# Optimization experiments

Hardware: AMD Instinct MI355X
Metric: run time of the kernel (lower is better)

Reference implementation:

```python
import jax, jax.numpy as jnp
import numpy as np

N = 8192
IN, HID, NH, TOT = 64, 64, 4, 128
DH = TOT // NH  # 32


def setup_inputs() -> dict:
    key = jax.random.key(0)
    ks = jax.random.split(key, 8)
    s = 0.05
    return {
        "input": jax.random.normal(ks[0], (N, IN), jnp.float32),
        "hx": jax.random.normal(ks[1], (N, HID), jnp.float32),
        "Wq": jax.random.normal(ks[2], (NH, TOT, DH), jnp.float32) * s,
        "Wk": jax.random.normal(ks[3], (NH, TOT, DH), jnp.float32) * s,
        "Wr": jax.random.normal(ks[4], (TOT, HID), jnp.float32) * s,
        "br": jnp.zeros((HID,), jnp.float32),
        "Wz": jax.random.normal(ks[5], (TOT, HID), jnp.float32) * s,
        "bz": jnp.zeros((HID,), jnp.float32),
        "Wh": jax.random.normal(ks[6], (TOT, HID), jnp.float32) * s,
        "bh": jnp.zeros((HID,), jnp.float32),
    }


def _dyn_adj(x, Wq, Wk):
    # x: [N, T]; multi-head attention adjacency, averaged over heads -> [N, N]
    q = jnp.einsum('nt,htd->hnd', x, Wq)
    k = jnp.einsum('nt,htd->hnd', x, Wk)
    scores = jnp.einsum('hnd,hmd->hnm', q, k) / jnp.sqrt(jnp.float32(DH))
    return jnp.mean(jax.nn.softmax(scores, axis=-1), axis=0)  # [N, N]


def reference(input, hx, Wq, Wk, Wr, br, Wz, bz, Wh, bh):
    x = jnp.concatenate([input, hx], axis=1)          # [N, TOT]
    adj = _dyn_adj(x, Wq, Wk)                         # [N, N] row-stochastic
    ax = adj @ x                                      # shared adjacency application
    r = jax.nn.sigmoid(ax @ Wr + br)                  # [N, HID]
    z = jax.nn.sigmoid(ax @ Wz + bz)                  # [N, HID]
    x2 = jnp.concatenate([input, r * hx], axis=1)     # [N, TOT]
    h = jnp.tanh((adj @ x2) @ Wh + bh)                # [N, HID]
    return z * hx + (1.0 - z) * h
```

## Files before the change

### kernel.cpp

```cpp
#include <hip/hip_runtime.h>
#include <hip/hip_bf16.h>

#define NN 8192
#define TOTD 128
#define HIDD 64
#define NHEAD 4
#define DHD 32
#define NCQ 8
#define JPB (NN / 32 / NCQ)

typedef __attribute__((ext_vector_type(8))) short short8;
typedef __attribute__((ext_vector_type(4))) float f32x4;

__device__ __forceinline__ short f2b(float f) {
  unsigned u = __builtin_bit_cast(unsigned, f);
  u += 0x7fff + ((u >> 16) & 1);
  return (short)(u >> 16);
}

__device__ __forceinline__ void gl_lds16(const short* g, short* l) {
  __builtin_amdgcn_global_load_lds(
      (const __attribute__((address_space(1))) void*)g,
      (__attribute__((address_space(3))) void*)l, 16, 0, 0);
}

__global__ void k_build_xfrag(const float* __restrict__ in, const float* __restrict__ hx,
                              short* __restrict__ xb) {
  int i = blockIdx.x * 256 + threadIdx.x;
  int n = i >> 7;
  int t = i & 127;
  float v = (t < 64) ? in[n * 64 + t] : hx[n * 64 + (t - 64)];
  int jt = n >> 5, kk = n & 31, cg = t >> 4;
  int l = ((kk >> 3) << 4) | (t & 15);
  xb[(((size_t)jt * 8 + cg) << 9) + (l << 3) + (kk & 7)] = f2b(v);
}

__global__ void k_qk(const float* __restrict__ in, const float* __restrict__ hx,
                     const float* __restrict__ Wq, const float* __restrict__ Wk,
                     short* __restrict__ qb, short* __restrict__ kb) {
  __shared__ float xr[TOTD];
  int n = blockIdx.x;
  int tid = threadIdx.x;
  if (tid < TOTD) xr[tid] = (tid < 64) ? in[n * 64 + tid] : hx[n * 64 + (tid - 64)];
  __syncthreads();
  int which = tid >> 7;
  int h = (tid >> 5) & 3;
  int d = tid & 31;
  const float* W = (which ? Wk : Wq) + h * TOTD * DHD + d;
  float acc = 0.f;
#pragma unroll
  for (int t = 0; t < TOTD; ++t) acc += xr[t] * W[t * DHD];
  int l = ((d >> 3) << 4) | (n & 15);
  if (!which) {
    acc *= 0.17677669529663687f;
    qb[(((size_t)(n >> 4) * 4 + h) << 9) + (l << 3) + (d & 7)] = f2b(acc);
  } else {
    kb[((((size_t)(n >> 5) * 4 + h) * 2 + ((n >> 4) & 1)) << 9) + (l << 3) + (d & 7)] = f2b(acc);
  }
}

__global__ __launch_bounds__(256, 4) void k_denom(
    const short* __restrict__ qb, const short* __restrict__ kb,
    float* __restrict__ lpart_g) {
  __shared__ short kbuf[2][8 * 512];
  const int tid = threadIdx.x;
  const int w = tid >> 6, l = tid & 63;
  const int row16 = l & 15, grp = l >> 4;
  const int r0 = blockIdx.x * 64 + w * 16;
  const int rtile = blockIdx.x * 4 + w;
  const int jt0 = blockIdx.y * JPB;
  const f32x4 zero4 = {0.f, 0.f, 0.f, 0.f};

  short8 qf[NHEAD];
#pragma unroll
  for (int h = 0; h < NHEAD; ++h)
    qf[h] = *(const short8*)&qb[(((size_t)rtile * 4 + h) << 9) + l * 8];

  float acc[NHEAD][4];
#pragma unroll
  for (int h = 0; h < NHEAD; ++h)
#pragma unroll
    for (int r = 0; r < 4; ++r) acc[h][r] = 0.f;

  for (int c = w; c < 8; c += 4)
    gl_lds16(kb + (((size_t)jt0 * 8 + c) << 9) + l * 8, &kbuf[0][c * 512]);
  __syncthreads();

  for (int j = 0; j < JPB; ++j) {
    int b = j & 1;
    if (j + 1 < JPB)
      for (int c = w; c < 8; c += 4)
        gl_lds16(kb + (((size_t)(jt0 + j + 1) * 8 + c) << 9) + l * 8, &kbuf[b ^ 1][c * 512]);
#pragma unroll
    for (int hs = 0; hs < 8; ++hs) {
      short8 kf = *(const short8*)&kbuf[b][hs * 512 + l * 8];
      f32x4 s = __builtin_amdgcn_mfma_f32_16x16x32_bf16(qf[hs >> 1], kf, zero4, 0, 0, 0);
#pragma unroll
      for (int r = 0; r < 4; ++r) acc[hs >> 1][r] += __expf(s[r]);
    }
    __syncthreads();
  }
#pragma unroll
  for (int m = 1; m < 16; m <<= 1)
#pragma unroll
    for (int h = 0; h < NHEAD; ++h)
#pragma unroll
      for (int r = 0; r < 4; ++r) acc[h][r] += __shfl_xor(acc[h][r], m, 64);

  if (row16 == 0) {
#pragma unroll
    for (int h = 0; h < NHEAD; ++h)
#pragma unroll
      for (int r = 0; r < 4; ++r)
        lpart_g[((size_t)blockIdx.y * NHEAD + h) * NN + r0 + grp * 4 + r] = acc[h][r];
  }
}

__global__ void k_linv(const float* __restrict__ lpart_g, float* __restrict__ linv_g) {
  int i = blockIdx.x * 256 + threadIdx.x;
  float s = 0.f;
#pragma unroll
  for (int q = 0; q < NCQ; ++q) s += lpart_g[(size_t)q * NHEAD * NN + i];
  linv_g[i] = 1.f / s;
}

__global__ __launch_bounds__(256, 4) void k_pv1(
    const short* __restrict__ qb, const short* __restrict__ kb,
    const short* __restrict__ xb, const float* __restrict__ linv_g,
    float* __restrict__ axq, short* __restrict__ Pf, int storeP) {
  __shared__ short kxbuf[2][16 * 512];
  __shared__ short Plds[4][16][32];
  const int tid = threadIdx.x;
  const int w = tid >> 6, l = tid & 63;
  const int row16 = l & 15, grp = l >> 4;
  const int r0 = blockIdx.x * 64 + w * 16;
  const int rtile = blockIdx.x * 4 + w;
  const int jt0 = blockIdx.y * JPB;
  const f32x4 zero4 = {0.f, 0.f, 0.f, 0.f};

  short8 qf[NHEAD];
#pragma unroll
  for (int h = 0; h < NHEAD; ++h)
    qf[h] = *(const short8*)&qb[(((size_t)rtile * 4 + h) << 9) + l * 8];
  float linv[NHEAD][4];
#pragma unroll
  for (int h = 0; h < NHEAD; ++h)
#pragma unroll
    for (int r = 0; r < 4; ++r) linv[h][r] = linv_g[h * NN + r0 + grp * 4 + r];

  f32x4 axa[8];
#pragma unroll
  for (int cg = 0; cg < 8; ++cg) axa[cg] = zero4;

  for (int c = w; c < 16; c += 4) {
    const short* src = (c < 8) ? kb + (((size_t)jt0 * 8 + c) << 9) + l * 8
                               : xb + (((size_t)jt0 * 8 + (c - 8)) << 9) + l * 8;
    gl_lds16(src, &kxbuf[0][c * 512]);
  }
  __syncthreads();

  for (int j = 0; j < JPB; ++j) {
    int b = j & 1;
    if (j + 1 < JPB) {
      for (int c = w; c < 16; c += 4) {
        const short* src = (c < 8) ? kb + (((size_t)(jt0 + j + 1) * 8 + c) << 9) + l * 8
                                   : xb + (((size_t)(jt0 + j + 1) * 8 + (c - 8)) << 9) + l * 8;
        gl_lds16(src, &kxbuf[b ^ 1][c * 512]);
      }
    }
    const short* kcur = kxbuf[b];
#pragma unroll
    for (int sub = 0; sub < 2; ++sub) {
      float p[4] = {0.f, 0.f, 0.f, 0.f};
#pragma unroll
      for (int h = 0; h < NHEAD; ++h) {
        short8 kf = *(const short8*)&kcur[(h * 2 + sub) * 512 + l * 8];
        f32x4 s = __builtin_amdgcn_mfma_f32_16x16x32_bf16(qf[h], kf, zero4, 0, 0, 0);
#pragma unroll
        for (int r = 0; r < 4; ++r) p[r] += __expf(s[r]) * linv[h][r];
      }
#pragma unroll
      for (int r = 0; r < 4; ++r)
        Plds[w][grp * 4 + r][sub * 16 + row16] = f2b(0.25f * p[r]);
    }
    short8 pa = *(short8*)&Plds[w][row16][grp * 8];
    if (storeP)
      *(short8*)&Pf[((size_t)rtile * 256 + (jt0 + j)) * 512 + l * 8] = pa;
#pragma unroll
    for (int cg = 0; cg < 8; ++cg) {
      short8 xv = *(const short8*)&kcur[(8 + cg) * 512 + l * 8];
      axa[cg] = __builtin_amdgcn_mfma_f32_16x16x32_bf16(pa, xv, axa[cg], 0, 0, 0);
    }
    __syncthreads();
  }
#pragma unroll
  for (int cg = 0; cg < 8; ++cg)
#pragma unroll
    for (int r = 0; r < 4; ++r)
      axq[(size_t)blockIdx.y * NN * TOTD + (size_t)(r0 + grp * 4 + r) * TOTD + cg * 16 + row16] =
          axa[cg][r];
}

__global__ void k_rz(const float* __restrict__ axq, const float* __restrict__ hx,
                     const float* __restrict__ Wr, const float* __restrict__ br,
                     const float* __restrict__ Wz, const float* __restrict__ bz,
                     float* __restrict__ ax, float* __restrict__ z,
                     short* __restrict__ v2f) {
  __shared__ float axs[2][TOTD];
  int tid = threadIdx.x;
  int rr = tid >> 7;
  int c2 = tid & 127;
  int n = blockIdx.x * 2 + rr;
  float s = 0.f;
#pragma unroll
  for (int q = 0; q < NCQ; ++q) s += axq[(size_t)q * NN * TOTD + (size_t)n * TOTD + c2];
  axs[rr][c2] = s;
  ax[(size_t)n * TOTD + c2] = s;
  __syncthreads();
  bool isz = c2 >= HIDD;
  int c = c2 & (HIDD - 1);
  const float* W = isz ? Wz : Wr;
  float acc = isz ? bz[c] : br[c];
#pragma unroll
  for (int t = 0; t < TOTD; ++t) acc += axs[rr][t] * W[t * HIDD + c];
  float sg = 1.f / (1.f + __expf(-acc));
  if (isz) {
    z[n * HIDD + c] = sg;
  } else {
    int jt = n >> 5, kk = n & 31, cg = c >> 4;
    int ll = ((kk >> 3) << 4) | (c & 15);
    v2f[(((size_t)jt * 4 + cg) << 9) + (ll << 3) + (kk & 7)] = f2b(sg * hx[n * HIDD + c]);
  }
}

__global__ __launch_bounds__(256, 4) void k_pv2P(
    const short* __restrict__ Pf, const short* __restrict__ v2f,
    float* __restrict__ a2q) {
  __shared__ short vbuf[2][4 * 512];
  const int tid = threadIdx.x;
  const int w = tid >> 6, l = tid & 63;
  const int row16 = l & 15, grp = l >> 4;
  const int r0 = blockIdx.x * 64 + w * 16;
  const int rtile = blockIdx.x * 4 + w;
  const int jt0 = blockIdx.y * JPB;

  f32x4 a2a[4];
#pragma unroll
  for (int cg = 0; cg < 4; ++cg) a2a[cg] = {0.f, 0.f, 0.f, 0.f};

  gl_lds16(v2f + (((size_t)jt0 * 4 + w) << 9) + l * 8, &vbuf[0][w * 512]);
  short8 pa = *(const short8*)&Pf[((size_t)rtile * 256 + jt0) * 512 + l * 8];
  __syncthreads();

  for (int j = 0; j < JPB; ++j) {
    int b = j & 1;
    short8 panext = pa;
    if (j + 1 < JPB) {
      gl_lds16(v2f + (((size_t)(jt0 + j + 1) * 4 + w) << 9) + l * 8, &vbuf[b ^ 1][w * 512]);
      panext = *(const short8*)&Pf[((size_t)rtile * 256 + (jt0 + j + 1)) * 512 + l * 8];
    }
#pragma unroll
    for (int cg = 0; cg < 4; ++cg) {
      short8 vv = *(const short8*)&vbuf[b][cg * 512 + l * 8];
      a2a[cg] = __builtin_amdgcn_mfma_f32_16x16x32_bf16(pa, vv, a2a[cg], 0, 0, 0);
    }
    pa = panext;
    __syncthreads();
  }
#pragma unroll
  for (int cg = 0; cg < 4; ++cg)
#pragma unroll
    for (int r = 0; r < 4; ++r)
      a2q[(size_t)blockIdx.y * NN * HIDD + (size_t)(r0 + grp * 4 + r) * HIDD + cg * 16 + row16] =
          a2a[cg][r];
}

__global__ __launch_bounds__(256, 4) void k_pv2R(
    const short* __restrict__ qb, const short* __restrict__ kb,
    const short* __restrict__ v2f, const float* __restrict__ linv_g,
    float* __restrict__ a2q) {
  __shared__ short kvbuf[2][12 * 512];
  __shared__ short Plds[4][16][32];
  const int tid = threadIdx.x;
  const int w = tid >> 6, l = tid & 63;
  const int row16 = l & 15, grp = l >> 4;
  const int r0 = blockIdx.x * 64 + w * 16;
  const int rtile = blockIdx.x * 4 + w;
  const int jt0 = blockIdx.y * JPB;
  const f32x4 zero4 = {0.f, 0.f, 0.f, 0.f};

  short8 qf[NHEAD];
#pragma unroll
  for (int h = 0; h < NHEAD; ++h)
    qf[h] = *(const short8*)&qb[(((size_t)rtile * 4 + h) << 9) + l * 8];
  float linv[NHEAD][4];
#pragma unroll
  for (int h = 0; h < NHEAD; ++h)
#pragma unroll
    for (int r = 0; r < 4; ++r) linv[h][r] = linv_g[h * NN + r0 + grp * 4 + r];

  f32x4 a2a[4];
#pragma unroll
  for (int cg = 0; cg < 4; ++cg) a2a[cg] = zero4;

  for (int c = w; c < 12; c += 4) {
    const short* src = (c < 8) ? kb + (((size_t)jt0 * 8 + c) << 9) + l * 8
                               : v2f + (((size_t)jt0 * 4 + (c - 8)) << 9) + l * 8;
    gl_lds16(src, &kvbuf[0][c * 512]);
  }
  __syncthreads();

  for (int j = 0; j < JPB; ++j) {
    int b = j & 1;
    if (j + 1 < JPB) {
      for (int c = w; c < 12; c += 4) {
        const short* src = (c < 8) ? kb + (((size_t)(jt0 + j + 1) * 8 + c) << 9) + l * 8
                                   : v2f + (((size_t)(jt0 + j + 1) * 4 + (c - 8)) << 9) + l * 8;
        gl_lds16(src, &kvbuf[b ^ 1][c * 512]);
      }
    }
    const short* kcur = kvbuf[b];
#pragma unroll
    for (int sub = 0; sub < 2; ++sub) {
      float p[4] = {0.f, 0.f, 0.f, 0.f};
#pragma unroll
      for (int h = 0; h < NHEAD; ++h) {
        short8 kf = *(const short8*)&kcur[(h * 2 + sub) * 512 + l * 8];
        f32x4 s = __builtin_amdgcn_mfma_f32_16x16x32_bf16(qf[h], kf, zero4, 0, 0, 0);
#pragma unroll
        for (int r = 0; r < 4; ++r) p[r] += __expf(s[r]) * linv[h][r];
      }
#pragma unroll
      for (int r = 0; r < 4; ++r)
        Plds[w][grp * 4 + r][sub * 16 + row16] = f2b(0.25f * p[r]);
    }
    short8 pa = *(short8*)&Plds[w][row16][grp * 8];
#pragma unroll
    for (int cg = 0; cg < 4; ++cg) {
      short8 vv = *(const short8*)&kcur[(8 + cg) * 512 + l * 8];
      a2a[cg] = __builtin_amdgcn_mfma_f32_16x16x32_bf16(pa, vv, a2a[cg], 0, 0, 0);
    }
    __syncthreads();
  }
#pragma unroll
  for (int cg = 0; cg < 4; ++cg)
#pragma unroll
    for (int r = 0; r < 4; ++r)
      a2q[(size_t)blockIdx.y * NN * HIDD + (size_t)(r0 + grp * 4 + r) * HIDD + cg * 16 + row16] =
          a2a[cg][r];
}

__global__ __launch_bounds__(256) void k_final(
    const float* __restrict__ a2q, const float* __restrict__ ax,
    const float* __restrict__ hx, const float* __restrict__ Wh,
    const float* __restrict__ bh, const float* __restrict__ z,
    float* __restrict__ out) {
  __shared__ float Whs[TOTD * HIDD];
  __shared__ float a2s[16][HIDD];
  const int tid = threadIdx.x;
  const int r0 = blockIdx.x * 16;

  for (int i = tid; i < TOTD * HIDD; i += 256) Whs[i] = Wh[i];
  for (int i = tid; i < 16 * HIDD; i += 256) {
    int rw = i >> 6, c = i & 63;
    size_t gi = (size_t)(r0 + rw) * HIDD + c;
    float s = 0.f;
#pragma unroll
    for (int q = 0; q < NCQ; ++q) s += a2q[(size_t)q * NN * HIDD + gi];
    a2s[rw][c] = s;
  }
  __syncthreads();
  for (int o = tid; o < 16 * HIDD; o += 256) {
    int rw = o >> 6, c = o & 63;
    const float* axrow = &ax[(size_t)(r0 + rw) * TOTD];
    float acc = bh[c];
#pragma unroll
    for (int t = 0; t < 64; ++t) acc += axrow[t] * Whs[t * HIDD + c];
#pragma unroll
    for (int t = 0; t < 64; ++t) acc += a2s[rw][t] * Whs[(64 + t) * HIDD + c];
    float hval = tanhf(acc);
    size_t gi = (size_t)(r0 + rw) * HIDD + c;
    float zz = z[gi];
    out[gi] = zz * hx[gi] + (1.f - zz) * hval;
  }
}

extern "C" void kernel_launch(void* const* d_in, const int* in_sizes, int n_in,
                              void* d_out, int out_size, void* d_ws, size_t ws_size,
                              hipStream_t stream) {
  const float* in = (const float*)d_in[0];
  const float* hx = (const float*)d_in[1];
  const float* Wq = (const float*)d_in[2];
  const float* Wk = (const float*)d_in[3];
  const float* Wr = (const float*)d_in[4];
  const float* br = (const float*)d_in[5];
  const float* Wz = (const float*)d_in[6];
  const float* bz = (const float*)d_in[7];
  const float* Wh = (const float*)d_in[8];
  const float* bh = (const float*)d_in[9];

  const size_t MB = 1ull << 20;
  char* ws = (char*)d_ws;
  short* qb    = (short*)(ws + 0 * MB);
  short* kb    = (short*)(ws + 2 * MB);
  short* xb    = (short*)(ws + 4 * MB);
  float* linv  = (float*)(ws + 6 * MB);
  float* lpart = (float*)(ws + 6 * MB + 262144);
  float* ax    = (float*)(ws + 8 * MB);
  float* z     = (float*)(ws + 12 * MB);
  short* v2f   = (short*)(ws + 14 * MB);
  float* axq   = (float*)(ws + 16 * MB);
  float* a2q   = (float*)(ws + 48 * MB);
  short* Pf    = (short*)(ws + 64 * MB);
  float* out   = (float*)d_out;
  int useP = (ws_size >= 192 * MB) ? 1 : 0;

  k_build_xfrag<<<dim3((NN * TOTD) / 256), dim3(256), 0, stream>>>(in, hx, xb);
  k_qk<<<dim3(NN), dim3(256), 0, stream>>>(in, hx, Wq, Wk, qb, kb);
  k_denom<<<dim3(NN / 64, NCQ), dim3(256), 0, stream>>>(qb, kb, lpart);
  k_linv<<<dim3((NHEAD * NN) / 256), dim3(256), 0, stream>>>(lpart, linv);
  k_pv1<<<dim3(NN / 64, NCQ), dim3(256), 0, stream>>>(qb, kb, xb, linv, axq, Pf, useP);
  k_rz<<<dim3(NN / 2), dim3(256), 0, stream>>>(axq, hx, Wr, br, Wz, bz, ax, z, v2f);
  if (useP)
    k_pv2P<<<dim3(NN / 64, NCQ), dim3(256), 0, stream>>>(Pf, v2f, a2q);
  else
    k_pv2R<<<dim3(NN / 64, NCQ), dim3(256), 0, stream>>>(qb, kb, v2f, linv, a2q);
  k_final<<<dim3(NN / 16), dim3(256), 0, stream>>>(a2q, ax, hx, Wh, bh, z, out);
}
```

Before: 221.5 us.

## Single-buffer LDS, raise occupancy, use exp2, recompute P instead of storing it

Several changes land together. The split-K factor goes from 8 to 16, and the attention kernels drop LDS double buffering to raise launch-bound occupancy. The log2(e) factor is folded into the Q scale so the kernels can call a native exp2, and the 0.25 head-average is folded into linv. The stored-P path for the second PV pass is removed, so P is always recomputed, and the padded Plds stride avoids bank conflicts. The changes trade prefetch overlap for more waves and less memory traffic, at the cost of more partial sums to reduce and slightly coarser bf16 rounding.

```diff
diff --git a/kernel.cpp b/kernel.cpp
--- a/kernel.cpp
+++ b/kernel.cpp
@@ -6,7 +6,7 @@
 #define HIDD 64
 #define NHEAD 4
 #define DHD 32
-#define NCQ 8
+#define NCQ 16
 #define JPB (NN / 32 / NCQ)
 
 typedef __attribute__((ext_vector_type(8))) short short8;
@@ -16,6 +16,17 @@
   unsigned u = __builtin_bit_cast(unsigned, f);
   u += 0x7fff + ((u >> 16) & 1);
   return (short)(u >> 16);
+}
+__device__ __forceinline__ short f2b_fast(float f) {
+  unsigned u = __builtin_bit_cast(unsigned, f);
+  return (short)((u + 0x8000u) >> 16);
+}
+__device__ __forceinline__ float fexp2(float x) {
+#if __has_builtin(__builtin_amdgcn_exp2f)
+  return __builtin_amdgcn_exp2f(x);
+#else
+  return exp2f(x);
+#endif
 }
 
 __device__ __forceinline__ void gl_lds16(const short* g, short* l) {
@@ -52,17 +63,17 @@
   for (int t = 0; t < TOTD; ++t) acc += xr[t] * W[t * DHD];
   int l = ((d >> 3) << 4) | (n & 15);
   if (!which) {
-    acc *= 0.17677669529663687f;
+    acc *= 0.25503486f;
     qb[(((size_t)(n >> 4) * 4 + h) << 9) + (l << 3) + (d & 7)] = f2b(acc);
   } else {
     kb[((((size_t)(n >> 5) * 4 + h) * 2 + ((n >> 4) & 1)) << 9) + (l << 3) + (d & 7)] = f2b(acc);
   }
 }
 
-__global__ __launch_bounds__(256, 4) void k_denom(
+__global__ __launch_bounds__(256, 8) void k_denom(
     const short* __restrict__ qb, const short* __restrict__ kb,
     float* __restrict__ lpart_g) {
-  __shared__ short kbuf[2][8 * 512];
+  __shared__ short kbuf[8 * 512];
   const int tid = threadIdx.x;
   const int w = tid >> 6, l = tid & 63;
   const int row16 = l & 15, grp = l >> 4;
@@ -82,21 +93,18 @@
 #pragma unroll
     for (int r = 0; r < 4; ++r) acc[h][r] = 0.f;
 
-  for (int c = w; c < 8; c += 4)
-    gl_lds16(kb + (((size_t)jt0 * 8 + c) << 9) + l * 8, &kbuf[0][c * 512]);
-  __syncthreads();
-
   for (int j = 0; j < JPB; ++j) {
-    int b = j & 1;
-    if (j + 1 < JPB)
-      for (int c = w; c < 8; c += 4)
-        gl_lds16(kb + (((size_t)(jt0 + j + 1) * 8 + c) << 9) + l * 8, &kbuf[b ^ 1][c * 512]);
+    int jt = jt0 + j;
+#pragma unroll
+    for (int c = w * 2; c < w * 2 + 2; ++c)
+      gl_lds16(kb + (((size_t)jt * 8 + c) << 9) + l * 8, &kbuf[c * 512]);
+    __syncthreads();
 #pragma unroll
     for (int hs = 0; hs < 8; ++hs) {
-      short8 kf = *(const short8*)&kbuf[b][hs * 512 + l * 8];
+      short8 kf = *(const short8*)&kbuf[hs * 512 + l * 8];
       f32x4 s = __builtin_amdgcn_mfma_f32_16x16x32_bf16(qf[hs >> 1], kf, zero4, 0, 0, 0);
 #pragma unroll
-      for (int r = 0; r < 4; ++r) acc[hs >> 1][r] += __expf(s[r]);
+      for (int r = 0; r < 4; ++r) acc[hs >> 1][r] += fexp2(s[r]);
     }
     __syncthreads();
   }
@@ -121,15 +129,15 @@
   float s = 0.f;
 #pragma unroll
   for (int q = 0; q < NCQ; ++q) s += lpart_g[(size_t)q * NHEAD * NN + i];
-  linv_g[i] = 1.f / s;
-}
-
-__global__ __launch_bounds__(256, 4) void k_pv1(
+  linv_g[i] = 0.25f / s;
+}
+
+__global__ __launch_bounds__(256, 5) void k_pv1(
     const short* __restrict__ qb, const short* __restrict__ kb,
     const short* __restrict__ xb, const float* __restrict__ linv_g,
-    float* __restrict__ axq, short* __restrict__ Pf, int storeP) {
-  __shared__ short kxbuf[2][16 * 512];
-  __shared__ short Plds[4][16][32];
+    float* __restrict__ axq) {
+  __shared__ short kxbuf[16 * 512];
+  __shared__ short Plds[4][16][40];
   const int tid = threadIdx.x;
   const int w = tid >> 6, l = tid & 63;
   const int row16 = l & 15, grp = l >> 4;
@@ -152,43 +160,33 @@
 #pragma unroll
   for (int cg = 0; cg < 8; ++cg) axa[cg] = zero4;
 
-  for (int c = w; c < 16; c += 4) {
-    const short* src = (c < 8) ? kb + (((size_t)jt0 * 8 + c) << 9) + l * 8
-                               : xb + (((size_t)jt0 * 8 + (c - 8)) << 9) + l * 8;
-    gl_lds16(src, &kxbuf[0][c * 512]);
-  }
-  __syncthreads();
-
   for (int j = 0; j < JPB; ++j) {
-    int b = j & 1;
-    if (j + 1 < JPB) {
-      for (int c = w; c < 16; c += 4) {
-        const short* src = (c < 8) ? kb + (((size_t)(jt0 + j + 1) * 8 + c) << 9) + l * 8
-                                   : xb + (((size_t)(jt0 + j + 1) * 8 + (c - 8)) << 9) + l * 8;
-        gl_lds16(src, &kxbuf[b ^ 1][c * 512]);
-      }
-    }
-    const short* kcur = kxbuf[b];
+    int jt = jt0 + j;
+#pragma unroll
+    for (int c = w * 4; c < w * 4 + 4; ++c) {
+      const short* src = (c < 8) ? kb + (((size_t)jt * 8 + c) << 9) + l * 8
+                                 : xb + (((size_t)jt * 8 + (c - 8)) << 9) + l * 8;
+      gl_lds16(src, &kxbuf[c * 512]);
+    }
+    __syncthreads();
 #pragma unroll
     for (int sub = 0; sub < 2; ++sub) {
       float p[4] = {0.f, 0.f, 0.f, 0.f};
 #pragma unroll
       for (int h = 0; h < NHEAD; ++h) {
-        short8 kf = *(const short8*)&kcur[(h * 2 + sub) * 512 + l * 8];
+        short8 kf = *(const short8*)&kxbuf[(h * 2 + sub) * 512 + l * 8];
         f32x4 s = __builtin_amdgcn_mfma_f32_16x16x32_bf16(qf[h], kf, zero4, 0, 0, 0);
 #pragma unroll
-        for (int r = 0; r < 4; ++r) p[r] += __expf(s[r]) * linv[h][r];
+        for (int r = 0; r < 4; ++r) p[r] += fexp2(s[r]) * linv[h][r];
       }
 #pragma unroll
       for (int r = 0; r < 4; ++r)
-        Plds[w][grp * 4 + r][sub * 16 + row16] = f2b(0.25f * p[r]);
+        Plds[w][grp * 4 + r][sub * 16 + row16] = f2b_fast(p[r]);
     }
     short8 pa = *(short8*)&Plds[w][row16][grp * 8];
-    if (storeP)
-      *(short8*)&Pf[((size_t)rtile * 256 + (jt0 + j)) * 512 + l * 8] = pa;
 #pragma unroll
     for (int cg = 0; cg < 8; ++cg) {
-      short8 xv = *(const short8*)&kcur[(8 + cg) * 512 + l * 8];
+      short8 xv = *(const short8*)&kxbuf[(8 + cg) * 512 + l * 8];
       axa[cg] = __builtin_amdgcn_mfma_f32_16x16x32_bf16(pa, xv, axa[cg], 0, 0, 0);
     }
     __syncthreads();
@@ -233,54 +231,12 @@
   }
 }
 
-__global__ __launch_bounds__(256, 4) void k_pv2P(
-    const short* __restrict__ Pf, const short* __restrict__ v2f,
-    float* __restrict__ a2q) {
-  __shared__ short vbuf[2][4 * 512];
-  const int tid = threadIdx.x;
-  const int w = tid >> 6, l = tid & 63;
-  const int row16 = l & 15, grp = l >> 4;
-  const int r0 = blockIdx.x * 64 + w * 16;
-  const int rtile = blockIdx.x * 4 + w;
-  const int jt0 = blockIdx.y * JPB;
-
-  f32x4 a2a[4];
-#pragma unroll
-  for (int cg = 0; cg < 4; ++cg) a2a[cg] = {0.f, 0.f, 0.f, 0.f};
-
-  gl_lds16(v2f + (((size_t)jt0 * 4 + w) << 9) + l * 8, &vbuf[0][w * 512]);
-  short8 pa = *(const short8*)&Pf[((size_t)rtile * 256 + jt0) * 512 + l * 8];
-  __syncthreads();
-
-  for (int j = 0; j < JPB; ++j) {
-    int b = j & 1;
-    short8 panext = pa;
-    if (j + 1 < JPB) {
-      gl_lds16(v2f + (((size_t)(jt0 + j + 1) * 4 + w) << 9) + l * 8, &vbuf[b ^ 1][w * 512]);
-      panext = *(const short8*)&Pf[((size_t)rtile * 256 + (jt0 + j + 1)) * 512 + l * 8];
-    }
-#pragma unroll
-    for (int cg = 0; cg < 4; ++cg) {
-      short8 vv = *(const short8*)&vbuf[b][cg * 512 + l * 8];
-      a2a[cg] = __builtin_amdgcn_mfma_f32_16x16x32_bf16(pa, vv, a2a[cg], 0, 0, 0);
-    }
-    pa = panext;
-    __syncthreads();
-  }
-#pragma unroll
-  for (int cg = 0; cg < 4; ++cg)
-#pragma unroll
-    for (int r = 0; r < 4; ++r)
-      a2q[(size_t)blockIdx.y * NN * HIDD + (size_t)(r0 + grp * 4 + r) * HIDD + cg * 16 + row16] =
-          a2a[cg][r];
-}
-
-__global__ __launch_bounds__(256, 4) void k_pv2R(
+__global__ __launch_bounds__(256, 5) void k_pv2(
     const short* __restrict__ qb, const short* __restrict__ kb,
     const short* __restrict__ v2f, const float* __restrict__ linv_g,
     float* __restrict__ a2q) {
-  __shared__ short kvbuf[2][12 * 512];
-  __shared__ short Plds[4][16][32];
+  __shared__ short kvbuf[12 * 512];
+  __shared__ short Plds[4][16][40];
   const int tid = threadIdx.x;
   const int w = tid >> 6, l = tid & 63;
   const int row16 = l & 15, grp = l >> 4;
@@ -303,41 +259,33 @@
 #pragma unroll
   for (int cg = 0; cg < 4; ++cg) a2a[cg] = zero4;
 
-  for (int c = w; c < 12; c += 4) {
-    const short* src = (c < 8) ? kb + (((size_t)jt0 * 8 + c) << 9) + l * 8
-                               : v2f + (((size_t)jt0 * 4 + (c - 8)) << 9) + l * 8;
-    gl_lds16(src, &kvbuf[0][c * 512]);
-  }
-  __syncthreads();
-
   for (int j = 0; j < JPB; ++j) {
-    int b = j & 1;
-    if (j + 1 < JPB) {
-      for (int c = w; c < 12; c += 4) {
-        const short* src = (c < 8) ? kb + (((size_t)(jt0 + j + 1) * 8 + c) << 9) + l * 8
-                                   : v2f + (((size_t)(jt0 + j + 1) * 4 + (c - 8)) << 9) + l * 8;
-        gl_lds16(src, &kvbuf[b ^ 1][c * 512]);
-      }
-    }
-    const short* kcur = kvbuf[b];
+    int jt = jt0 + j;
+#pragma unroll
+    for (int c = w * 3; c < w * 3 + 3; ++c) {
+      const short* src = (c < 8) ? kb + (((size_t)jt * 8 + c) << 9) + l * 8
+                                 : v2f + (((size_t)jt * 4 + (c - 8)) << 9) + l * 8;
+      gl_lds16(src, &kvbuf[c * 512]);
+    }
+    __syncthreads();
 #pragma unroll
     for (int sub = 0; sub < 2; ++sub) {
       float p[4] = {0.f, 0.f, 0.f, 0.f};
 #pragma unroll
       for (int h = 0; h < NHEAD; ++h) {
-        short8 kf = *(const short8*)&kcur[(h * 2 + sub) * 512 + l * 8];
+        short8 kf = *(const short8*)&kvbuf[(h * 2 + sub) * 512 + l * 8];
         f32x4 s = __builtin_amdgcn_mfma_f32_16x16x32_bf16(qf[h], kf, zero4, 0, 0, 0);
 #pragma unroll
-        for (int r = 0; r < 4; ++r) p[r] += __expf(s[r]) * linv[h][r];
+        for (int r = 0; r < 4; ++r) p[r] += fexp2(s[r]) * linv[h][r];
       }
 #pragma unroll
       for (int r = 0; r < 4; ++r)
-        Plds[w][grp * 4 + r][sub * 16 + row16] = f2b(0.25f * p[r]);
+        Plds[w][grp * 4 + r][sub * 16 + row16] = f2b_fast(p[r]);
     }
     short8 pa = *(short8*)&Plds[w][row16][grp * 8];
 #pragma unroll
     for (int cg = 0; cg < 4; ++cg) {
-      short8 vv = *(const short8*)&kcur[(8 + cg) * 512 + l * 8];
+      short8 vv = *(const short8*)&kvbuf[(8 + cg) * 512 + l * 8];
       a2a[cg] = __builtin_amdgcn_mfma_f32_16x16x32_bf16(pa, vv, a2a[cg], 0, 0, 0);
     }
     __syncthreads();
@@ -405,25 +353,20 @@
   short* kb    = (short*)(ws + 2 * MB);
   short* xb    = (short*)(ws + 4 * MB);
   float* linv  = (float*)(ws + 6 * MB);
-  float* lpart = (float*)(ws + 6 * MB + 262144);
-  float* ax    = (float*)(ws + 8 * MB);
-  float* z     = (float*)(ws + 12 * MB);
-  short* v2f   = (short*)(ws + 14 * MB);
-  float* axq   = (float*)(ws + 16 * MB);
-  float* a2q   = (float*)(ws + 48 * MB);
-  short* Pf    = (short*)(ws + 64 * MB);
+  float* lpart = (float*)(ws + 7 * MB);
+  float* ax    = (float*)(ws + 10 * MB);
+  float* z     = (float*)(ws + 14 * MB);
+  short* v2f   = (short*)(ws + 16 * MB);
+  float* axq   = (float*)(ws + 20 * MB);
+  float* a2q   = (float*)(ws + 84 * MB);
   float* out   = (float*)d_out;
-  int useP = (ws_size >= 192 * MB) ? 1 : 0;
 
   k_build_xfrag<<<dim3((NN * TOTD) / 256), dim3(256), 0, stream>>>(in, hx, xb);
   k_qk<<<dim3(NN), dim3(256), 0, stream>>>(in, hx, Wq, Wk, qb, kb);
   k_denom<<<dim3(NN / 64, NCQ), dim3(256), 0, stream>>>(qb, kb, lpart);
   k_linv<<<dim3((NHEAD * NN) / 256), dim3(256), 0, stream>>>(lpart, linv);
-  k_pv1<<<dim3(NN / 64, NCQ), dim3(256), 0, stream>>>(qb, kb, xb, linv, axq, Pf, useP);
+  k_pv1<<<dim3(NN / 64, NCQ), dim3(256), 0, stream>>>(qb, kb, xb, linv, axq);
   k_rz<<<dim3(NN / 2), dim3(256), 0, stream>>>(axq, hx, Wr, br, Wz, bz, ax, z, v2f);
-  if (useP)
-    k_pv2P<<<dim3(NN / 64, NCQ), dim3(256), 0, stream>>>(Pf, v2f, a2q);
-  else
-    k_pv2R<<<dim3(NN / 64, NCQ), dim3(256), 0, stream>>>(qb, kb, v2f, linv, a2q);
+  k_pv2<<<dim3(NN / 64, NCQ), dim3(256), 0, stream>>>(qb, kb, v2f, linv, a2q);
   k_final<<<dim3(NN / 16), dim3(256), 0, stream>>>(a2q, ax, hx, Wh, bh, z, out);
 }
```

After: 239.1 us. 1.08x slower.
